# Optimization experiments

Measured on AMD Instinct MI355X. Metric: run time of the kernel, lower is better.

Reference implementation:

```python
import jax, jax.numpy as jnp
import numpy as np

N_HEAD = 8


def setup_inputs() -> dict:
    key = jax.random.key(0)
    ks = jax.random.split(key, 5)
    D = 512
    q = jax.random.normal(ks[0], (2, 4096, D), dtype=jnp.float32)
    s = 0.02  # init scale for weights
    Wq = jax.random.normal(ks[1], (D, D), dtype=jnp.float32) * s
    Wk = jax.random.normal(ks[2], (D, D), dtype=jnp.float32) * s
    Wv = jax.random.normal(ks[3], (D, D), dtype=jnp.float32) * s
    Wo = jax.random.normal(ks[4], (D, D), dtype=jnp.float32) * s
    z = jnp.zeros((D,), dtype=jnp.float32)
    return {"q": q, "Wq": Wq, "bq": z, "Wk": Wk, "bk": z, "Wv": Wv, "bv": z, "Wo": Wo, "bo": z}


def _split_heads(x, n_head):
    # (b, s, c) -> (b, h, s, c//h)
    b, s, c = x.shape
    return x.reshape(b, s, n_head, c // n_head).transpose(0, 2, 1, 3)


def reference(q, Wq, bq, Wk, bk, Wv, bv, Wo, bo):
    # Linear projections (nn.Linear: x @ W.T + b); self-attention (kv = q)
    qp = _split_heads(q @ Wq.T + bq, N_HEAD)  # (b, h, s, dh)
    kp = _split_heads(q @ Wk.T + bk, N_HEAD)
    vp = _split_heads(q @ Wv.T + bv, N_HEAD)
    dh = qp.shape[-1]
    scale = 1.0 / jnp.sqrt(jnp.asarray(dh, dtype=qp.dtype))
    # unfused MATH-backend SDPA: full [b,h,s,s] scores, stable softmax, no dropout (eval)
    scores = jnp.einsum("bhqd,bhkd->bhqk", qp, kp) * scale
    probs = jax.nn.softmax(scores, axis=-1)
    attn = jnp.einsum("bhqk,bhkd->bhqd", probs, vp)  # (b, h, s, dh)
    # merge heads: (b, h, s, dh) -> (b, s, h*dh)
    b, h, s, _ = attn.shape
    merged = attn.transpose(0, 2, 1, 3).reshape(b, s, h * dh)
    return merged @ Wo.T + bo
```

## Files before the change

### kernel.cpp

```cpp
#include <hip/hip_runtime.h>
#include <hip/hip_bf16.h>
#include <math.h>

typedef __attribute__((ext_vector_type(8))) short bf16x8;
typedef __attribute__((ext_vector_type(4))) short bf16x4;
typedef __attribute__((ext_vector_type(4))) float f32x4;

__device__ __forceinline__ unsigned short f2bf(float f) {
    union { float f; unsigned int u; } v; v.f = f;
    unsigned int u = v.u;
    u += 0x7fffu + ((u >> 16) & 1u);
    return (unsigned short)(u >> 16);
}

__device__ __forceinline__ f32x4 mfma16(bf16x4 a, bf16x4 b, f32x4 c) {
#if __has_builtin(__builtin_amdgcn_mfma_f32_16x16x16bf16_1k)
    return __builtin_amdgcn_mfma_f32_16x16x16bf16_1k(a, b, c, 0, 0, 0);
#else
    asm volatile("v_mfma_f32_16x16x16_bf16 %0, %1, %2, %0\n\ts_nop 7"
                 : "+v"(c) : "v"(a), "v"(b));
    return c;
#endif
}

__device__ __forceinline__ unsigned packbf2(float a, float b) {
    __hip_bfloat162 h = __float22bfloat162_rn(float2{a, b});
    union { __hip_bfloat162 h; unsigned u; } v; v.h = h;
    return v.u;
}

__device__ __forceinline__ float fmax3(float a, float b, float c) {
    return fmaxf(fmaxf(a, b), c);
}

template<int A_BF16>
__device__ __forceinline__ void gemm_body(const void* Ap, const float* W,
                                          f32x4 (&acc)[4][4],
                                          unsigned short (*As)[40], unsigned short (*Bs)[40],
                                          int bm, int bn, int t)
{
    constexpr int Kdim = 512;
    const int lane = t & 63, g = lane >> 4, c = lane & 15;
    const int w = t >> 6, wr = w >> 1, wc = w & 1;

    uint4  paB[2];
    float4 paF[4];
    float4 pw[4];
    const int ccB = (t & 3) * 8, r0B = t >> 2;
    const int c4  = (t & 7) * 4, r0F = t >> 3;

    if (A_BF16) {
        const unsigned short* A = (const unsigned short*)Ap;
        for (int p = 0; p < 2; ++p)
            paB[p] = *(const uint4*)(A + (size_t)(bm + r0B + p * 64) * Kdim + ccB);
    } else {
        const float* A = (const float*)Ap;
        for (int p = 0; p < 4; ++p)
            paF[p] = *(const float4*)(A + (size_t)(bm + r0F + p * 32) * Kdim + c4);
    }
    for (int p = 0; p < 4; ++p)
        pw[p] = *(const float4*)(W + (size_t)(bn + r0F + p * 32) * Kdim + c4);

    for (int k0 = 0; k0 < Kdim; k0 += 32) {
        __syncthreads();
        if (A_BF16) {
            for (int p = 0; p < 2; ++p)
                *(uint4*)&As[r0B + p * 64][ccB] = paB[p];
        } else {
            for (int p = 0; p < 4; ++p) {
                float4 v = paF[p];
                ushort4 hv;
                hv.x = f2bf(v.x); hv.y = f2bf(v.y); hv.z = f2bf(v.z); hv.w = f2bf(v.w);
                *(ushort4*)&As[r0F + p * 32][c4] = hv;
            }
        }
        for (int p = 0; p < 4; ++p) {
            float4 v = pw[p];
            ushort4 hv;
            hv.x = f2bf(v.x); hv.y = f2bf(v.y); hv.z = f2bf(v.z); hv.w = f2bf(v.w);
            *(ushort4*)&Bs[r0F + p * 32][c4] = hv;
        }
        __syncthreads();
        if (k0 + 32 < Kdim) {
            const int kn = k0 + 32;
            if (A_BF16) {
                const unsigned short* A = (const unsigned short*)Ap;
                for (int p = 0; p < 2; ++p)
                    paB[p] = *(const uint4*)(A + (size_t)(bm + r0B + p * 64) * Kdim + kn + ccB);
            } else {
                const float* A = (const float*)Ap;
                for (int p = 0; p < 4; ++p)
                    paF[p] = *(const float4*)(A + (size_t)(bm + r0F + p * 32) * Kdim + kn + c4);
            }
            for (int p = 0; p < 4; ++p)
                pw[p] = *(const float4*)(W + (size_t)(bn + r0F + p * 32) * Kdim + kn + c4);
        }
        bf16x8 af[4], bfr[4];
        for (int i = 0; i < 4; ++i)
            af[i] = *(const bf16x8*)&As[wr * 64 + i * 16 + c][g * 8];
        for (int j = 0; j < 4; ++j)
            bfr[j] = *(const bf16x8*)&Bs[wc * 64 + j * 16 + c][g * 8];
        for (int i = 0; i < 4; ++i)
            for (int j = 0; j < 4; ++j)
                acc[i][j] = __builtin_amdgcn_mfma_f32_16x16x32_bf16(af[i], bfr[j], acc[i][j], 0, 0, 0);
    }
}

__global__ __launch_bounds__(256, 2)
void gemm_qkv(const float* __restrict__ q,
              const float* __restrict__ Wq, const float* __restrict__ bq,
              const float* __restrict__ Wk, const float* __restrict__ bk,
              const float* __restrict__ Wv, const float* __restrict__ bv,
              unsigned short* __restrict__ Qo, unsigned short* __restrict__ Ko,
              unsigned short* __restrict__ Vo)
{
    __shared__ unsigned short As[128][40];
    __shared__ unsigned short Bs[128][40];
    const int t = threadIdx.x, z = blockIdx.z;
    const int lane = t & 63, g = lane >> 4, c = lane & 15;
    const int w = t >> 6, wr = w >> 1, wc = w & 1;
    const int bm = blockIdx.x * 128, bn = blockIdx.y * 128;

    const float* W    = (z == 0) ? Wq : (z == 1) ? Wk : Wv;
    const float* bias = (z == 0) ? bq : (z == 1) ? bk : bv;
    unsigned short* Out = (z == 0) ? Qo : (z == 1) ? Ko : Vo;
    const float osc = (z == 0) ? 0.125f * 1.44269504f : 1.0f;

    f32x4 acc[4][4] = {};
    gemm_body<0>((const void*)q, W, acc, As, Bs, bm, bn, t);

    float bv4[4];
    for (int j = 0; j < 4; ++j) bv4[j] = bias[bn + wc * 64 + j * 16 + c];
    for (int i = 0; i < 4; ++i)
        for (int j = 0; j < 4; ++j)
            for (int r = 0; r < 4; ++r) {
                int m = bm + wr * 64 + i * 16 + 4 * g + r;
                int n = bn + wc * 64 + j * 16 + c;
                float val = (acc[i][j][r] + bv4[j]) * osc;
                int b = m >> 12, s = m & 4095, h = n >> 6, d = n & 63;
                if (z < 2)
                    Out[((((size_t)b * 8 + h) * 4096 + s) << 6) + d] = f2bf(val);
                else
                    Out[(((size_t)b * 8 + h) * 64 + d) * 4096 + s] = f2bf(val);
            }
}

__global__ __launch_bounds__(256, 2)
void gemm_out(const unsigned short* __restrict__ A, const float* __restrict__ W,
              const float* __restrict__ bias, float* __restrict__ Out)
{
    __shared__ unsigned short As[128][40];
    __shared__ unsigned short Bs[128][40];
    const int t = threadIdx.x;
    const int lane = t & 63, g = lane >> 4, c = lane & 15;
    const int w = t >> 6, wr = w >> 1, wc = w & 1;
    const int bm = blockIdx.x * 128, bn = blockIdx.y * 128;

    f32x4 acc[4][4] = {};
    gemm_body<1>((const void*)A, W, acc, As, Bs, bm, bn, t);

    float bv4[4];
    for (int j = 0; j < 4; ++j) bv4[j] = bias[bn + wc * 64 + j * 16 + c];
    for (int i = 0; i < 4; ++i)
        for (int j = 0; j < 4; ++j)
            for (int r = 0; r < 4; ++r) {
                int m = bm + wr * 64 + i * 16 + 4 * g + r;
                int n = bn + wc * 64 + j * 16 + c;
                Out[(size_t)m * 512 + n] = acc[i][j][r] + bv4[j];
            }
}

__global__ __launch_bounds__(512, 4)
void attn128(const unsigned short* __restrict__ Q, const unsigned short* __restrict__ Kh,
             const unsigned short* __restrict__ VT, unsigned short* __restrict__ Mo)
{
    __shared__ unsigned short Ks[2 * 128 * 64];
    __shared__ unsigned short Vs[2 * 64 * 128];

    const int t = threadIdx.x, w = t >> 6, lane = t & 63, g = lane >> 4, c = lane & 15;
    const int idp = (blockIdx.x & 7) * 64 + (blockIdx.x >> 3);
    const int bh = idp >> 5;
    const int q0 = (idp & 31) * 128;
    const unsigned short* Qb = Q + (size_t)bh * 4096 * 64;
    const unsigned short* Kb = Kh + (size_t)bh * 4096 * 64;
    const unsigned short* Vb = VT + (size_t)bh * 64 * 4096;

    bf16x8 qf0, qf1;
    {
        int qr = q0 + w * 16 + c;
        qf0 = *(const bf16x8*)(Qb + (size_t)qr * 64 + g * 8);
        qf1 = *(const bf16x8*)(Qb + (size_t)qr * 64 + 32 + g * 8);
    }

    f32x4 o[4] = {};
    f32x4 lacc = {};
    float nm = 0.f;

    bf16x4 ones;
    ones[0] = ones[1] = ones[2] = ones[3] = (short)0x3F80;

    const int srow = t >> 3, s0 = t & 7;
    const int scol = s0 * 8, r7 = srow & 7;
    const int woffK  = srow * 64 + ((s0 ^ r7) << 3);
    const int woffKB = (64 + srow) * 64 + ((s0 ^ r7) << 3);
    const int woffV  = srow * 128 + ((s0 ^ r7) << 3);
    const int woffVB = srow * 128 + ((8 + (s0 ^ r7)) << 3);
    const unsigned short* kpA = Kb + (size_t)srow * 64 + scol;
    const unsigned short* vpA = Vb + (size_t)srow * 4096 + scol;

    uint4 kaA = *(const uint4*)(kpA);
    uint4 kaB = *(const uint4*)(kpA + 64 * 64);
    uint4 vaA = *(const uint4*)(vpA);
    uint4 vaB = *(const uint4*)(vpA + 64);
    *(uint4*)&Ks[woffK]  = kaA;
    *(uint4*)&Ks[woffKB] = kaB;
    *(uint4*)&Vs[woffV]  = vaA;
    *(uint4*)&Vs[woffVB] = vaB;

    const float THR = 10.f;
    const int c7 = c & 7;

    auto half_iter = [&](const unsigned short* Kc, const unsigned short* Vc, int h8) {
        f32x4 ta[4];
        __builtin_amdgcn_s_setprio(1);
        #pragma unroll
        for (int nt = 0; nt < 4; ++nt) {
            int row = nt * 16 + c;
            bf16x8 kf0 = *(const bf16x8*)&Kc[row * 64 + ((g ^ c7) << 3)];
            bf16x8 kf1 = *(const bf16x8*)&Kc[row * 64 + (((4 + g) ^ c7) << 3)];
            f32x4 z = {nm, nm, nm, nm};
            z = __builtin_amdgcn_mfma_f32_16x16x32_bf16(kf0, qf0, z, 0, 0, 0);
            z = __builtin_amdgcn_mfma_f32_16x16x32_bf16(kf1, qf1, z, 0, 0, 0);
            ta[nt] = z;
        }
        __builtin_amdgcn_s_setprio(0);

        float tm = fmax3(fmax3(fmax3(ta[0][0], ta[0][1], ta[0][2]),
                               fmax3(ta[0][3], ta[1][0], ta[1][1]),
                               fmax3(ta[1][2], ta[1][3], ta[2][0])),
                         fmax3(ta[2][1], ta[2][2], ta[2][3]),
                         fmax3(fmax3(ta[3][0], ta[3][1], ta[3][2]), ta[3][3], ta[3][3]));
        if (!__all(tm <= THR)) {
            float pm = tm;
            pm = fmaxf(pm, __shfl_xor(pm, 16));
            pm = fmaxf(pm, __shfl_xor(pm, 32));
            float dm = fmaxf(pm, 0.f);
            nm -= dm;
            float al = exp2f(-dm);
            #pragma unroll
            for (int nt = 0; nt < 4; ++nt)
                #pragma unroll
                for (int r = 0; r < 4; ++r) ta[nt][r] -= dm;
            #pragma unroll
            for (int r = 0; r < 4; ++r) {
                float ar = __shfl(al, 4 * g + r);
                #pragma unroll
                for (int nd = 0; nd < 4; ++nd) o[nd][r] *= ar;
                lacc[r] *= ar;
            }
        }

        __builtin_amdgcn_s_setprio(1);
        #pragma unroll
        for (int nt = 0; nt < 4; ++nt) {
            union { unsigned u[2]; bf16x4 v; } pk;
            pk.u[0] = packbf2(exp2f(ta[nt][0]), exp2f(ta[nt][1]));
            pk.u[1] = packbf2(exp2f(ta[nt][2]), exp2f(ta[nt][3]));
            bf16x4 pfn = pk.v;
            #pragma unroll
            for (int nd = 0; nd < 4; ++nd) {
                int row = nd * 16 + c;
                int off = row * 128 + ((h8 + ((2 * nt + (g >> 1)) ^ c7)) << 3) + ((g & 1) << 2);
                bf16x4 vf = *(const bf16x4*)&Vc[off];
                o[nd] = mfma16(pfn, vf, o[nd]);
            }
            lacc = mfma16(pfn, ones, lacc);
        }
        __builtin_amdgcn_s_setprio(0);
    };

    auto tile_iter = [&](int it, const unsigned short* Kc, const unsigned short* Vc,
                         unsigned short* Kn, unsigned short* Vn) {
        __syncthreads();
        if (it < 31) {
            const unsigned short* kp = kpA + (size_t)(it + 1) * 8192;
            const unsigned short* vp = vpA + (it + 1) * 128;
            kaA = *(const uint4*)(kp);
            kaB = *(const uint4*)(kp + 64 * 64);
            vaA = *(const uint4*)(vp);
            vaB = *(const uint4*)(vp + 64);
        }
        if (w & 1) {
            half_iter(Kc + 64 * 64, Vc, 8);
            half_iter(Kc, Vc, 0);
        } else {
            half_iter(Kc, Vc, 0);
            half_iter(Kc + 64 * 64, Vc, 8);
        }
        if (it < 31) {
            *(uint4*)&Kn[woffK]  = kaA;
            *(uint4*)&Kn[woffKB] = kaB;
            *(uint4*)&Vn[woffV]  = vaA;
            *(uint4*)&Vn[woffVB] = vaB;
        }
    };

    for (int it2 = 0; it2 < 32; it2 += 2) {
        tile_iter(it2,     &Ks[0],    &Vs[0],    &Ks[8192], &Vs[8192]);
        tile_iter(it2 + 1, &Ks[8192], &Vs[8192], &Ks[0],    &Vs[0]);
    }

    const int b = bh >> 3, h = bh & 7;
    #pragma unroll
    for (int r = 0; r < 4; ++r) {
        float inv = 1.f / lacc[r];
        int m = b * 4096 + q0 + w * 16 + 4 * g + r;
        #pragma unroll
        for (int nd = 0; nd < 4; ++nd) {
            int n = h * 64 + nd * 16 + c;
            Mo[(size_t)m * 512 + n] = f2bf(o[nd][r] * inv);
        }
    }
}

extern "C" void kernel_launch(void* const* d_in, const int* in_sizes, int n_in,
                              void* d_out, int out_size, void* d_ws, size_t ws_size,
                              hipStream_t stream) {
    const float* q  = (const float*)d_in[0];
    const float* Wq = (const float*)d_in[1];
    const float* bq = (const float*)d_in[2];
    const float* Wk = (const float*)d_in[3];
    const float* bk = (const float*)d_in[4];
    const float* Wv = (const float*)d_in[5];
    const float* bv = (const float*)d_in[6];
    const float* Wo = (const float*)d_in[7];
    const float* bo = (const float*)d_in[8];

    unsigned short* Qb = (unsigned short*)d_ws;
    unsigned short* Kb = Qb + (size_t)16 * 4096 * 64;
    unsigned short* Vt = Kb + (size_t)16 * 4096 * 64;
    unsigned short* Mg = Vt + (size_t)16 * 4096 * 64;

    dim3 gb(256);
    dim3 gqkv(64, 4, 3);
    gemm_qkv<<<gqkv, gb, 0, stream>>>(q, Wq, bq, Wk, bk, Wv, bv, Qb, Kb, Vt);

    dim3 ga(512), gba(512);
    attn128<<<ga, gba, 0, stream>>>(Qb, Kb, Vt, Mg);

    dim3 gg(64, 4);
    gemm_out<<<gg, gb, 0, stream>>>(Mg, Wo, bo, (float*)d_out);
}
```

Before: 173.7 us.

## Switch attention to 32x32x16 MFMA with 256-row query tiles per block

Rewrites the attention kernel to use 32x32x16 bf16 MFMA instructions, with each wave owning 32 query rows. Each block now covers 256 queries and the grid halves to 256 blocks. The probability fragments are rearranged into the P·V operand layout with v_permlane32_swap rather than going through LDS. This is meant to cut MFMA instruction count and LDS traffic per FLOP and to double K/V tile reuse across queries. In exchange it uses more registers, sets launch bounds to 2 blocks per SM, and leaves fewer blocks to fill the GPU.

```diff
diff --git a/kernel.cpp b/kernel.cpp
--- a/kernel.cpp
+++ b/kernel.cpp
@@ -3,8 +3,8 @@
 #include <math.h>
 
 typedef __attribute__((ext_vector_type(8))) short bf16x8;
-typedef __attribute__((ext_vector_type(4))) short bf16x4;
 typedef __attribute__((ext_vector_type(4))) float f32x4;
+typedef __attribute__((ext_vector_type(16))) float f32x16;
 
 __device__ __forceinline__ unsigned short f2bf(float f) {
     union { float f; unsigned int u; } v; v.f = f;
@@ -13,20 +13,18 @@
     return (unsigned short)(u >> 16);
 }
 
-__device__ __forceinline__ f32x4 mfma16(bf16x4 a, bf16x4 b, f32x4 c) {
-#if __has_builtin(__builtin_amdgcn_mfma_f32_16x16x16bf16_1k)
-    return __builtin_amdgcn_mfma_f32_16x16x16bf16_1k(a, b, c, 0, 0, 0);
-#else
-    asm volatile("v_mfma_f32_16x16x16_bf16 %0, %1, %2, %0\n\ts_nop 7"
-                 : "+v"(c) : "v"(a), "v"(b));
-    return c;
-#endif
+__device__ __forceinline__ f32x16 mfma32(bf16x8 a, bf16x8 b, f32x16 c) {
+    return __builtin_amdgcn_mfma_f32_32x32x16_bf16(a, b, c, 0, 0, 0);
 }
 
 __device__ __forceinline__ unsigned packbf2(float a, float b) {
     __hip_bfloat162 h = __float22bfloat162_rn(float2{a, b});
     union { __hip_bfloat162 h; unsigned u; } v; v.h = h;
     return v.u;
+}
+
+__device__ __forceinline__ void pl32swap(unsigned &a, unsigned &b) {
+    asm volatile("v_permlane32_swap_b32 %0, %1" : "+v"(a), "+v"(b));
 }
 
 __device__ __forceinline__ float fmax3(float a, float b, float c) {
@@ -170,34 +168,44 @@
             }
 }
 
-__global__ __launch_bounds__(512, 4)
-void attn128(const unsigned short* __restrict__ Q, const unsigned short* __restrict__ Kh,
+__global__ __launch_bounds__(512, 2)
+void attn256(const unsigned short* __restrict__ Q, const unsigned short* __restrict__ Kh,
              const unsigned short* __restrict__ VT, unsigned short* __restrict__ Mo)
 {
     __shared__ unsigned short Ks[2 * 128 * 64];
     __shared__ unsigned short Vs[2 * 64 * 128];
 
-    const int t = threadIdx.x, w = t >> 6, lane = t & 63, g = lane >> 4, c = lane & 15;
-    const int idp = (blockIdx.x & 7) * 64 + (blockIdx.x >> 3);
-    const int bh = idp >> 5;
-    const int q0 = (idp & 31) * 128;
+    const int t = threadIdx.x, w = t >> 6, l = t & 63;
+    const int l5 = l >> 5, c31 = l & 31;
+    const int idp = (blockIdx.x & 7) * 32 + (blockIdx.x >> 3);
+    const int bh = idp >> 4;
+    const int q0 = (idp & 15) * 256;
     const unsigned short* Qb = Q + (size_t)bh * 4096 * 64;
     const unsigned short* Kb = Kh + (size_t)bh * 4096 * 64;
     const unsigned short* Vb = VT + (size_t)bh * 64 * 4096;
 
-    bf16x8 qf0, qf1;
-    {
-        int qr = q0 + w * 16 + c;
-        qf0 = *(const bf16x8*)(Qb + (size_t)qr * 64 + g * 8);
-        qf1 = *(const bf16x8*)(Qb + (size_t)qr * 64 + 32 + g * 8);
-    }
-
-    f32x4 o[4] = {};
-    f32x4 lacc = {};
+    const int qr = q0 + w * 32 + c31;
+    bf16x8 qv0 = *(const bf16x8*)(Qb + (size_t)qr * 64 + 8 * l5);
+    bf16x8 qv1 = *(const bf16x8*)(Qb + (size_t)qr * 64 + 16 + 8 * l5);
+    bf16x8 qv2 = *(const bf16x8*)(Qb + (size_t)qr * 64 + 32 + 8 * l5);
+    bf16x8 qv3 = *(const bf16x8*)(Qb + (size_t)qr * 64 + 48 + 8 * l5);
+
+    f32x16 o0 = {}, o1 = {}, lac = {};
     float nm = 0.f;
 
-    bf16x4 ones;
-    ones[0] = ones[1] = ones[2] = ones[3] = (short)0x3F80;
+    bf16x8 ones;
+    #pragma unroll
+    for (int i = 0; i < 8; ++i) ones[i] = (short)0x3F80;
+
+    const int sl01 = (l5 ^ (l & 1)) * 8;
+    const int ka0 = c31 * 64 + (0 ^ (l & 6)) * 8 + sl01;
+    const int ka1 = c31 * 64 + (2 ^ (l & 6)) * 8 + sl01;
+    const int ka2 = c31 * 64 + (4 ^ (l & 6)) * 8 + sl01;
+    const int ka3 = c31 * 64 + (6 ^ (l & 6)) * 8 + sl01;
+    const int va0 = c31 * 128 + (0 ^ (l & 6)) * 8 + sl01;
+    const int va1 = c31 * 128 + (2 ^ (l & 6)) * 8 + sl01;
+    const int va2 = c31 * 128 + (4 ^ (l & 6)) * 8 + sl01;
+    const int va3 = c31 * 128 + (6 ^ (l & 6)) * 8 + sl01;
 
     const int srow = t >> 3, s0 = t & 7;
     const int scol = s0 * 8, r7 = srow & 7;
@@ -218,69 +226,90 @@
     *(uint4*)&Vs[woffVB] = vaB;
 
     const float THR = 10.f;
-    const int c7 = c & 7;
-
-    auto half_iter = [&](const unsigned short* Kc, const unsigned short* Vc, int h8) {
-        f32x4 ta[4];
+
+    auto half_iter = [&](int kbase, int vbase) {
+        f32x16 ta, tb;
         __builtin_amdgcn_s_setprio(1);
+        {
+            f32x16 z = {nm, nm, nm, nm, nm, nm, nm, nm, nm, nm, nm, nm, nm, nm, nm, nm};
+            z = mfma32(*(const bf16x8*)&Ks[kbase + ka0], qv0, z);
+            z = mfma32(*(const bf16x8*)&Ks[kbase + ka1], qv1, z);
+            z = mfma32(*(const bf16x8*)&Ks[kbase + ka2], qv2, z);
+            z = mfma32(*(const bf16x8*)&Ks[kbase + ka3], qv3, z);
+            ta = z;
+        }
+        {
+            f32x16 z = {nm, nm, nm, nm, nm, nm, nm, nm, nm, nm, nm, nm, nm, nm, nm, nm};
+            z = mfma32(*(const bf16x8*)&Ks[kbase + 2048 + ka0], qv0, z);
+            z = mfma32(*(const bf16x8*)&Ks[kbase + 2048 + ka1], qv1, z);
+            z = mfma32(*(const bf16x8*)&Ks[kbase + 2048 + ka2], qv2, z);
+            z = mfma32(*(const bf16x8*)&Ks[kbase + 2048 + ka3], qv3, z);
+            tb = z;
+        }
+        __builtin_amdgcn_s_setprio(0);
+
+        float tm = -3.0e38f;
         #pragma unroll
-        for (int nt = 0; nt < 4; ++nt) {
-            int row = nt * 16 + c;
-            bf16x8 kf0 = *(const bf16x8*)&Kc[row * 64 + ((g ^ c7) << 3)];
-            bf16x8 kf1 = *(const bf16x8*)&Kc[row * 64 + (((4 + g) ^ c7) << 3)];
-            f32x4 z = {nm, nm, nm, nm};
-            z = __builtin_amdgcn_mfma_f32_16x16x32_bf16(kf0, qf0, z, 0, 0, 0);
-            z = __builtin_amdgcn_mfma_f32_16x16x32_bf16(kf1, qf1, z, 0, 0, 0);
-            ta[nt] = z;
-        }
-        __builtin_amdgcn_s_setprio(0);
-
-        float tm = fmax3(fmax3(fmax3(ta[0][0], ta[0][1], ta[0][2]),
-                               fmax3(ta[0][3], ta[1][0], ta[1][1]),
-                               fmax3(ta[1][2], ta[1][3], ta[2][0])),
-                         fmax3(ta[2][1], ta[2][2], ta[2][3]),
-                         fmax3(fmax3(ta[3][0], ta[3][1], ta[3][2]), ta[3][3], ta[3][3]));
+        for (int i = 0; i < 16; ++i) tm = fmax3(tm, ta[i], tb[i]);
         if (!__all(tm <= THR)) {
-            float pm = tm;
-            pm = fmaxf(pm, __shfl_xor(pm, 16));
-            pm = fmaxf(pm, __shfl_xor(pm, 32));
+            float pm = fmaxf(tm, __shfl_xor(tm, 32));
             float dm = fmaxf(pm, 0.f);
             nm -= dm;
             float al = exp2f(-dm);
             #pragma unroll
-            for (int nt = 0; nt < 4; ++nt)
-                #pragma unroll
-                for (int r = 0; r < 4; ++r) ta[nt][r] -= dm;
+            for (int i = 0; i < 16; ++i) { ta[i] -= dm; tb[i] -= dm; }
             #pragma unroll
-            for (int r = 0; r < 4; ++r) {
-                float ar = __shfl(al, 4 * g + r);
-                #pragma unroll
-                for (int nd = 0; nd < 4; ++nd) o[nd][r] *= ar;
-                lacc[r] *= ar;
-            }
+            for (int i = 0; i < 16; ++i) {
+                float ar = __shfl(al, (i & 3) + 8 * (i >> 2));
+                o0[i] *= ar; o1[i] *= ar; lac[i] *= ar;
+            }
+        }
+
+        union { unsigned u[4]; bf16x8 v; } p0, p1, p2, p3;
+        {
+            unsigned x0 = packbf2(exp2f(ta[0]),  exp2f(ta[1]));
+            unsigned x1 = packbf2(exp2f(ta[2]),  exp2f(ta[3]));
+            unsigned y0 = packbf2(exp2f(ta[4]),  exp2f(ta[5]));
+            unsigned y1 = packbf2(exp2f(ta[6]),  exp2f(ta[7]));
+            pl32swap(x0, y0); pl32swap(x1, y1);
+            p0.u[0] = x0; p0.u[1] = x1; p0.u[2] = y0; p0.u[3] = y1;
+            x0 = packbf2(exp2f(ta[8]),  exp2f(ta[9]));
+            x1 = packbf2(exp2f(ta[10]), exp2f(ta[11]));
+            y0 = packbf2(exp2f(ta[12]), exp2f(ta[13]));
+            y1 = packbf2(exp2f(ta[14]), exp2f(ta[15]));
+            pl32swap(x0, y0); pl32swap(x1, y1);
+            p1.u[0] = x0; p1.u[1] = x1; p1.u[2] = y0; p1.u[3] = y1;
+            x0 = packbf2(exp2f(tb[0]),  exp2f(tb[1]));
+            x1 = packbf2(exp2f(tb[2]),  exp2f(tb[3]));
+            y0 = packbf2(exp2f(tb[4]),  exp2f(tb[5]));
+            y1 = packbf2(exp2f(tb[6]),  exp2f(tb[7]));
+            pl32swap(x0, y0); pl32swap(x1, y1);
+            p2.u[0] = x0; p2.u[1] = x1; p2.u[2] = y0; p2.u[3] = y1;
+            x0 = packbf2(exp2f(tb[8]),  exp2f(tb[9]));
+            x1 = packbf2(exp2f(tb[10]), exp2f(tb[11]));
+            y0 = packbf2(exp2f(tb[12]), exp2f(tb[13]));
+            y1 = packbf2(exp2f(tb[14]), exp2f(tb[15]));
+            pl32swap(x0, y0); pl32swap(x1, y1);
+            p3.u[0] = x0; p3.u[1] = x1; p3.u[2] = y0; p3.u[3] = y1;
         }
 
         __builtin_amdgcn_s_setprio(1);
-        #pragma unroll
-        for (int nt = 0; nt < 4; ++nt) {
-            union { unsigned u[2]; bf16x4 v; } pk;
-            pk.u[0] = packbf2(exp2f(ta[nt][0]), exp2f(ta[nt][1]));
-            pk.u[1] = packbf2(exp2f(ta[nt][2]), exp2f(ta[nt][3]));
-            bf16x4 pfn = pk.v;
-            #pragma unroll
-            for (int nd = 0; nd < 4; ++nd) {
-                int row = nd * 16 + c;
-                int off = row * 128 + ((h8 + ((2 * nt + (g >> 1)) ^ c7)) << 3) + ((g & 1) << 2);
-                bf16x4 vf = *(const bf16x4*)&Vc[off];
-                o[nd] = mfma16(pfn, vf, o[nd]);
-            }
-            lacc = mfma16(pfn, ones, lacc);
-        }
+        o0  = mfma32(p0.v, *(const bf16x8*)&Vs[vbase + va0], o0);
+        o1  = mfma32(p0.v, *(const bf16x8*)&Vs[vbase + 4096 + va0], o1);
+        lac = mfma32(p0.v, ones, lac);
+        o0  = mfma32(p1.v, *(const bf16x8*)&Vs[vbase + va1], o0);
+        o1  = mfma32(p1.v, *(const bf16x8*)&Vs[vbase + 4096 + va1], o1);
+        lac = mfma32(p1.v, ones, lac);
+        o0  = mfma32(p2.v, *(const bf16x8*)&Vs[vbase + va2], o0);
+        o1  = mfma32(p2.v, *(const bf16x8*)&Vs[vbase + 4096 + va2], o1);
+        lac = mfma32(p2.v, ones, lac);
+        o0  = mfma32(p3.v, *(const bf16x8*)&Vs[vbase + va3], o0);
+        o1  = mfma32(p3.v, *(const bf16x8*)&Vs[vbase + 4096 + va3], o1);
+        lac = mfma32(p3.v, ones, lac);
         __builtin_amdgcn_s_setprio(0);
     };
 
-    auto tile_iter = [&](int it, const unsigned short* Kc, const unsigned short* Vc,
-                         unsigned short* Kn, unsigned short* Vn) {
+    auto tile_iter = [&](int it, int kb, int vb) {
         __syncthreads();
         if (it < 31) {
             const unsigned short* kp = kpA + (size_t)(it + 1) * 8192;
@@ -290,36 +319,30 @@
             vaA = *(const uint4*)(vp);
             vaB = *(const uint4*)(vp + 64);
         }
-        if (w & 1) {
-            half_iter(Kc + 64 * 64, Vc, 8);
-            half_iter(Kc, Vc, 0);
-        } else {
-            half_iter(Kc, Vc, 0);
-            half_iter(Kc + 64 * 64, Vc, 8);
-        }
+        half_iter(kb, vb);
+        half_iter(kb + 4096, vb + 64);
         if (it < 31) {
-            *(uint4*)&Kn[woffK]  = kaA;
-            *(uint4*)&Kn[woffKB] = kaB;
-            *(uint4*)&Vn[woffV]  = vaA;
-            *(uint4*)&Vn[woffVB] = vaB;
+            int ko = kb ^ 8192, vo = vb ^ 8192;
+            *(uint4*)&Ks[ko + woffK]  = kaA;
+            *(uint4*)&Ks[ko + woffKB] = kaB;
+            *(uint4*)&Vs[vo + woffV]  = vaA;
+            *(uint4*)&Vs[vo + woffVB] = vaB;
         }
     };
 
     for (int it2 = 0; it2 < 32; it2 += 2) {
-        tile_iter(it2,     &Ks[0],    &Vs[0],    &Ks[8192], &Vs[8192]);
-        tile_iter(it2 + 1, &Ks[8192], &Vs[8192], &Ks[0],    &Vs[0]);
+        tile_iter(it2, 0, 0);
+        tile_iter(it2 + 1, 8192, 8192);
     }
 
     const int b = bh >> 3, h = bh & 7;
     #pragma unroll
-    for (int r = 0; r < 4; ++r) {
-        float inv = 1.f / lacc[r];
-        int m = b * 4096 + q0 + w * 16 + 4 * g + r;
-        #pragma unroll
-        for (int nd = 0; nd < 4; ++nd) {
-            int n = h * 64 + nd * 16 + c;
-            Mo[(size_t)m * 512 + n] = f2bf(o[nd][r] * inv);
-        }
+    for (int i = 0; i < 16; ++i) {
+        int qrow = (i & 3) + 8 * (i >> 2) + 4 * l5;
+        float inv = 1.f / lac[i];
+        size_t m = (size_t)(b * 4096 + q0 + w * 32 + qrow) * 512 + h * 64 + c31;
+        Mo[m]      = f2bf(o0[i] * inv);
+        Mo[m + 32] = f2bf(o1[i] * inv);
     }
 }
 
@@ -345,8 +368,7 @@
     dim3 gqkv(64, 4, 3);
     gemm_qkv<<<gqkv, gb, 0, stream>>>(q, Wq, bq, Wk, bk, Wv, bv, Qb, Kb, Vt);
 
-    dim3 ga(512), gba(512);
-    attn128<<<ga, gba, 0, stream>>>(Qb, Kb, Vt, Mg);
+    attn256<<<dim3(256), dim3(512), 0, stream>>>(Qb, Kb, Vt, Mg);
 
     dim3 gg(64, 4);
     gemm_out<<<gg, gb, 0, stream>>>(Mg, Wo, bo, (float*)d_out);
```

After: 174.3 us. Within noise of the previous version (+0.4%).
